# Performance work log

Measured on AMD Instinct MI355X. Metric: run time of the kernel, lower is better.

## Reference

```python
import jax, jax.numpy as jnp
import numpy as np
import math

HIDDEN = 2048
HEADS = 16
GROUPS = 4
HEAD_DIM = HIDDEN // HEADS  # 128
KV_DIM = GROUPS * HEAD_DIM  # 512
B, S = 2, 2048


def setup_inputs() -> dict:
    key = jax.random.key(0)
    ks = jax.random.split(key, 10)
    scale = 0.02
    return {
        "X": jax.random.normal(ks[0], (B, S, HIDDEN), dtype=jnp.float32),
        "attention_mask": jnp.ones((B, S), dtype=jnp.int32),
        "Wq": jax.random.normal(ks[1], (HIDDEN, HIDDEN), dtype=jnp.float32) * scale,
        "bq": jnp.zeros((HIDDEN,), dtype=jnp.float32),
        "Wk": jax.random.normal(ks[2], (HIDDEN, KV_DIM), dtype=jnp.float32) * scale,
        "bk": jnp.zeros((KV_DIM,), dtype=jnp.float32),
        "Wv": jax.random.normal(ks[3], (HIDDEN, KV_DIM), dtype=jnp.float32) * scale,
        "bv": jnp.zeros((KV_DIM,), dtype=jnp.float32),
        "Wo": jax.random.normal(ks[4], (HIDDEN, HIDDEN), dtype=jnp.float32) * scale,
        "bo": jnp.zeros((HIDDEN,), dtype=jnp.float32),
    }


def reference(X, attention_mask, Wq, bq, Wk, bk, Wv, bv, Wo, bo):
    b, s, _ = X.shape
    num_per_group = HEADS // GROUPS
    # projections
    Q = (X @ Wq + bq).reshape(b, s, HEADS, HEAD_DIM).transpose(0, 2, 1, 3)   # [b,H,s,d]
    K = (X @ Wk + bk).reshape(b, s, GROUPS, HEAD_DIM).transpose(0, 2, 1, 3)  # [b,G,s,d]
    V = (X @ Wv + bv).reshape(b, s, GROUPS, HEAD_DIM).transpose(0, 2, 1, 3)
    # torch .repeat(1, num_per_group, 1, 1) tiles group axis: [g0..gG-1, g0..gG-1, ...]
    K = jnp.tile(K, (1, num_per_group, 1, 1))  # [b,H,s,d]
    V = jnp.tile(V, (1, num_per_group, 1, 1))
    scores = jnp.einsum("bhqd,bhkd->bhqk", Q, K) / math.sqrt(HEAD_DIM)
    mask = attention_mask[:, None, None, :] == 0  # [b,1,1,s]
    scores = jnp.where(mask, jnp.float32(-jnp.inf), scores)
    attn = jax.nn.softmax(scores, axis=-1)
    out = jnp.einsum("bhqk,bhkd->bhqd", attn, V)  # [b,H,s,d]
    out = out.transpose(0, 2, 1, 3).reshape(b, s, HIDDEN)
    return out @ Wo + bo
```

## Files before the change

### kernel.cpp

```cpp
#include <hip/hip_runtime.h>
#include <hip/hip_bf16.h>


typedef __attribute__((ext_vector_type(8))) short short8;
typedef __attribute__((ext_vector_type(4))) short short4v;
typedef __attribute__((ext_vector_type(4))) float float4v;

#define C1F 0.12751743f
#define B0F -16.0f

#if defined(__has_builtin) && __has_builtin(__builtin_amdgcn_exp2f)
#define EXP2(x) __builtin_amdgcn_exp2f(x)
#else
#define EXP2(x) exp2f(x)
#endif

__device__ __forceinline__ short f2bf(float x) {
    __hip_bfloat16 h = __float2bfloat16(x);
    short s; __builtin_memcpy(&s, &h, sizeof(s)); return s;
}

__device__ __forceinline__ void gl16(const short* g, short* l) {
    __builtin_amdgcn_global_load_lds(
        (const __attribute__((address_space(1))) void*)g,
        (__attribute__((address_space(3))) void*)l, 16, 0, 0);
}

__global__ __launch_bounds__(256) void cvt_bf16_kernel(const float* __restrict__ in,
                                                       short* __restrict__ out, int n) {
    int i = (blockIdx.x * 256 + threadIdx.x) * 4;
    if (i >= n) return;
    float4 v = *(const float4*)(in + i);
    short4v o;
    o[0] = f2bf(v.x); o[1] = f2bf(v.y); o[2] = f2bf(v.z); o[3] = f2bf(v.w);
    *(short4v*)(out + i) = o;
}

__global__ __launch_bounds__(256) void transpose_cvt_kernel(const float* __restrict__ W,
                                                            short* __restrict__ Wt,
                                                            int K, int N) {
    __shared__ float tile[32][33];
    int n0 = blockIdx.x * 32, k0 = blockIdx.y * 32;
    int tx = threadIdx.x & 31, ty = threadIdx.x >> 5;
#pragma unroll
    for (int i = 0; i < 4; ++i) {
        int kk = ty + i * 8;
        tile[kk][tx] = W[(size_t)(k0 + kk) * N + n0 + tx];
    }
    __syncthreads();
#pragma unroll
    for (int i = 0; i < 4; ++i) {
        int nn = ty + i * 8;
        Wt[(size_t)(n0 + nn) * K + k0 + tx] = f2bf(tile[tx][nn]);
    }
}

__global__ __launch_bounds__(256) void gemm_dma_kernel(
    const short* __restrict__ A, const short* __restrict__ Bt,
    const float* __restrict__ b0, const float* __restrict__ b1, const float* __restrict__ b2,
    short* __restrict__ O0, short* __restrict__ O1, short* __restrict__ O2,
    float* __restrict__ Of, int K, int mode) {
    __shared__ short As[128 * 32];
    __shared__ short Bs[128 * 32];
    const int t = threadIdx.x, lane = t & 63, w = t >> 6;
    const int l15 = lane & 15, quad = lane >> 4;
    const int wm = (w & 1) * 64, wn = (w >> 1) * 64;
    const int m0 = blockIdx.y * 128, n0 = blockIdx.x * 128;
    const int r4 = lane >> 2, c8 = (lane & 3) * 8;
    const short* ga = A + (size_t)(m0 + w * 16 + r4) * K + c8;
    const short* gb = Bt + (size_t)(n0 + w * 16 + r4) * K + c8;
    short* lA = As + (w * 16) * 32;
    short* lB = Bs + (w * 16) * 32;

    float4v acc[4][4] = {};

    for (int k0 = 0; k0 < K; k0 += 32) {
        gl16(ga + k0, lA);
        gl16(ga + (size_t)64 * K + k0, lA + 64 * 32);
        gl16(gb + k0, lB);
        gl16(gb + (size_t)64 * K + k0, lB + 64 * 32);
        __syncthreads();
        short8 af[4], bfr[4];
#pragma unroll
        for (int i = 0; i < 4; ++i)
            af[i] = *(const short8*)(As + (wm + i * 16 + l15) * 32 + quad * 8);
#pragma unroll
        for (int j = 0; j < 4; ++j)
            bfr[j] = *(const short8*)(Bs + (wn + j * 16 + l15) * 32 + quad * 8);
#pragma unroll
        for (int i = 0; i < 4; ++i)
#pragma unroll
            for (int j = 0; j < 4; ++j)
                acc[i][j] = __builtin_amdgcn_mfma_f32_16x16x32_bf16(af[i], bfr[j], acc[i][j], 0, 0, 0);
        __syncthreads();
    }

#pragma unroll
    for (int i = 0; i < 4; ++i) {
#pragma unroll
        for (int j = 0; j < 4; ++j) {
            const int col = n0 + wn + j * 16 + l15;
            const int row0 = m0 + wm + i * 16 + quad * 4;
            if (mode == 1) {
                const float bc = b0[col];
#pragma unroll
                for (int r = 0; r < 4; ++r)
                    Of[(size_t)(row0 + r) * 2048 + col] = acc[i][j][r] + bc;
            } else if (col < 2048) {
                const float bc = b0[col];
#pragma unroll
                for (int r = 0; r < 4; ++r)
                    O0[(size_t)(row0 + r) * 2048 + col] = f2bf(acc[i][j][r] + bc);
            } else if (col < 2560) {
                const int c = col - 2048;
                const float bc = b1[c];
#pragma unroll
                for (int r = 0; r < 4; ++r)
                    O1[(size_t)(row0 + r) * 512 + c] = f2bf(acc[i][j][r] + bc);
            } else {
                const int c = col - 2560;
                const float bc = b2[c];
#pragma unroll
                for (int r = 0; r < 4; ++r)
                    O2[(size_t)c * 4096 + row0 + r] = f2bf(acc[i][j][r] + bc);
            }
        }
    }
}

__global__ __launch_bounds__(256, 2) void flash_kernel(
    const short* __restrict__ Qb, const short* __restrict__ Kb,
    const short* __restrict__ Vt, const int* __restrict__ mask,
    short* __restrict__ Ab) {
    __shared__ short Ks[64 * 136];
    __shared__ short Vs[128 * 72];
    __shared__ short Ps[4 * 32 * 72];
    __shared__ float mb[64];

    const int t = threadIdx.x;
    const int lane = t & 63, w = t >> 6;
    const int l15 = lane & 15, quad = lane >> 4;
    const int qt = blockIdx.x, g = blockIdx.y, b = blockIdx.z;
    const int h = g + 4 * w;
    const int q0 = qt * 32;

    short8 qf[2][4];
#pragma unroll
    for (int mi = 0; mi < 2; ++mi)
#pragma unroll
        for (int ks = 0; ks < 4; ++ks)
            qf[mi][ks] = *(const short8*)(Qb + (size_t)(b * 2048 + q0 + mi * 16 + l15) * 2048
                                          + h * 128 + ks * 32 + quad * 8);

    float4v o[2][8] = {};
    float rsum[2][4] = {};
    short* PsW = Ps + w * (32 * 72);
    const int psxr = ((l15 >> 3) & 1) << 4;

    const int kR = t >> 4, kC = (t & 15) * 8;
    const int vR = t >> 3, vC = (t & 7) * 8;
    const short* kg = Kb + (size_t)(b * 2048 + kR) * 512 + g * 128 + kC;
    const short* vg = Vt + (size_t)(g * 128 + vR) * 4096 + (size_t)b * 2048 + vC;

    short8 kv[4], vv[4];
    float mv = 0.f;

#define LOADT(KB)                                                                  \
    do {                                                                           \
        kv[0] = *(const short8*)(kg + (size_t)(KB) * 512);                         \
        kv[1] = *(const short8*)(kg + (size_t)((KB) + 16) * 512);                  \
        kv[2] = *(const short8*)(kg + (size_t)((KB) + 32) * 512);                  \
        kv[3] = *(const short8*)(kg + (size_t)((KB) + 48) * 512);                  \
        vv[0] = *(const short8*)(vg + (KB));                                       \
        vv[1] = *(const short8*)(vg + (size_t)32 * 4096 + (KB));                   \
        vv[2] = *(const short8*)(vg + (size_t)64 * 4096 + (KB));                   \
        vv[3] = *(const short8*)(vg + (size_t)96 * 4096 + (KB));                   \
        if (t < 64) mv = mask[b * 2048 + (KB) + t] ? B0F : -1e30f;                 \
    } while (0)

    LOADT(0);

    for (int kt = 0; kt < 32; ++kt) {
        __syncthreads();
#pragma unroll
        for (int i = 0; i < 4; ++i)
            *(short8*)(Ks + (kR + i * 16) * 136 + kC) = kv[i];
#pragma unroll
        for (int i = 0; i < 4; ++i)
            *(short8*)(Vs + (vR + i * 32) * 72 + vC) = vv[i];
        if (t < 64) mb[t] = mv;
        __syncthreads();

        if (kt + 1 < 32) LOADT((kt + 1) * 64);

        float4v s[2][4] = {};
        __builtin_amdgcn_s_setprio(1);
#pragma unroll
        for (int ks = 0; ks < 4; ++ks)
#pragma unroll
            for (int j = 0; j < 4; ++j) {
                short8 bk = *(const short8*)(Ks + (j * 16 + l15) * 136 + ks * 32 + quad * 8);
                s[0][j] = __builtin_amdgcn_mfma_f32_16x16x32_bf16(qf[0][ks], bk, s[0][j], 0, 0, 0);
                s[1][j] = __builtin_amdgcn_mfma_f32_16x16x32_bf16(qf[1][ks], bk, s[1][j], 0, 0, 0);
            }
        __builtin_amdgcn_s_setprio(0);
#pragma unroll
        for (int mi = 0; mi < 2; ++mi)
#pragma unroll
            for (int j = 0; j < 4; ++j) {
                const float mbias = mb[j * 16 + l15];
#pragma unroll
                for (int r = 0; r < 4; ++r) {
                    float p = EXP2(fmaf(s[mi][j][r], C1F, mbias));
                    rsum[mi][r] += p;
                    const int row = mi * 16 + quad * 4 + r;
                    PsW[row * 72 + ((j * 16 + l15) ^ (((row >> 3) & 1) << 4))] = f2bf(p);
                }
            }
        __builtin_amdgcn_s_setprio(1);
#pragma unroll
        for (int ks2 = 0; ks2 < 2; ++ks2) {
            short8 pa0 = *(const short8*)(PsW + l15 * 72 + ((ks2 * 32 + quad * 8) ^ psxr));
            short8 pa1 = *(const short8*)(PsW + (16 + l15) * 72 + ((ks2 * 32 + quad * 8) ^ psxr));
#pragma unroll
            for (int jj = 0; jj < 8; ++jj) {
                short8 bv = *(const short8*)(Vs + (jj * 16 + l15) * 72 + ks2 * 32 + quad * 8);
                o[0][jj] = __builtin_amdgcn_mfma_f32_16x16x32_bf16(pa0, bv, o[0][jj], 0, 0, 0);
                o[1][jj] = __builtin_amdgcn_mfma_f32_16x16x32_bf16(pa1, bv, o[1][jj], 0, 0, 0);
            }
        }
        __builtin_amdgcn_s_setprio(0);
    }
#undef LOADT

    float rinv[2][4];
#pragma unroll
    for (int mi = 0; mi < 2; ++mi)
#pragma unroll
        for (int r = 0; r < 4; ++r) {
            float v = rsum[mi][r];
            v += __shfl_xor(v, 1, 64); v += __shfl_xor(v, 2, 64);
            v += __shfl_xor(v, 4, 64); v += __shfl_xor(v, 8, 64);
            rinv[mi][r] = (v > 0.f) ? 1.f / v : 0.f;
        }
    const size_t ob = (size_t)(b * 2048 + q0) * 2048 + h * 128;
#pragma unroll
    for (int mi = 0; mi < 2; ++mi)
#pragma unroll
        for (int jj = 0; jj < 8; ++jj)
#pragma unroll
            for (int r = 0; r < 4; ++r)
                Ab[ob + (size_t)(mi * 16 + quad * 4 + r) * 2048 + jj * 16 + l15] =
                    f2bf(o[mi][jj][r] * rinv[mi][r]);
}

extern "C" void kernel_launch(void* const* d_in, const int* in_sizes, int n_in,
                              void* d_out, int out_size, void* d_ws, size_t ws_size,
                              hipStream_t stream) {
    (void)in_sizes; (void)n_in; (void)out_size; (void)ws_size;
    const float* X  = (const float*)d_in[0];
    const int* mask = (const int*)d_in[1];
    const float* Wq = (const float*)d_in[2];
    const float* bq = (const float*)d_in[3];
    const float* Wk = (const float*)d_in[4];
    const float* bk = (const float*)d_in[5];
    const float* Wv = (const float*)d_in[6];
    const float* bv = (const float*)d_in[7];
    const float* Wo = (const float*)d_in[8];
    const float* bo = (const float*)d_in[9];
    float* out = (float*)d_out;

    char* ws = (char*)d_ws;
    short* Xb     = (short*)(ws + 0);
    short* WqkvT  = (short*)(ws + 16777216);
    short* Wot    = (short*)(ws + 29360128);
    short* Qb     = (short*)(ws + 37748736);
    short* Kb     = (short*)(ws + 54525952);
    short* Vt     = (short*)(ws + 58720256);
    short* Ab     = Xb;

    const int M = 4096, HID = 2048, KV = 512;

    cvt_bf16_kernel<<<8192, 256, 0, stream>>>(X, Xb, M * HID);
    transpose_cvt_kernel<<<dim3(64, 64), 256, 0, stream>>>(Wq, WqkvT, HID, HID);
    transpose_cvt_kernel<<<dim3(16, 64), 256, 0, stream>>>(Wk, WqkvT + (size_t)2048 * 2048, HID, KV);
    transpose_cvt_kernel<<<dim3(16, 64), 256, 0, stream>>>(Wv, WqkvT + (size_t)2560 * 2048, HID, KV);
    transpose_cvt_kernel<<<dim3(64, 64), 256, 0, stream>>>(Wo, Wot, HID, HID);

    gemm_dma_kernel<<<dim3(24, 32), 256, 0, stream>>>(
        Xb, WqkvT, bq, bk, bv, Qb, Kb, Vt, nullptr, HID, 0);

    flash_kernel<<<dim3(64, 4, 2), 256, 0, stream>>>(Qb, Kb, Vt, mask, Ab);

    gemm_dma_kernel<<<dim3(16, 32), 256, 0, stream>>>(
        Ab, Wot, bo, nullptr, nullptr, nullptr, nullptr, nullptr, out, HID, 1);
}
```

Measured before the change: 355.6 us.

## Rewrite flash attention with 32x32 MFMA, register-resident P, double-buffered LDS

The attention kernel moves from 16x16x32 to 32x32x16 bf16 MFMA and computes S transposed, so the softmax probabilities stay in registers and feed the PV MFMA directly instead of passing through an LDS scratch buffer. K/V tiles are double-buffered in LDS, which drops one barrier per iteration. The mask becomes a wave ballot bitmask applied with selects. The projection epilogue writes V transposed in a permuted row order so it matches the new P register layout. The cost is more LDS for the second buffer and a heavier accumulator register footprint.

```diff
diff --git a/kernel.cpp b/kernel.cpp
--- a/kernel.cpp
+++ b/kernel.cpp
@@ -5,6 +5,7 @@
 typedef __attribute__((ext_vector_type(8))) short short8;
 typedef __attribute__((ext_vector_type(4))) short short4v;
 typedef __attribute__((ext_vector_type(4))) float float4v;
+typedef __attribute__((ext_vector_type(16))) float float16v;
 
 #define C1F 0.12751743f
 #define B0F -16.0f
@@ -120,9 +121,11 @@
             } else {
                 const int c = col - 2560;
                 const float bc = b2[c];
+                const int qsw = ((quad & 1) << 1) | (quad >> 1);
+                const int prow = m0 + wm + i * 16 + qsw * 4;
 #pragma unroll
                 for (int r = 0; r < 4; ++r)
-                    O2[(size_t)c * 4096 + row0 + r] = f2bf(acc[i][j][r] + bc);
+                    O2[(size_t)c * 4096 + prow + r] = f2bf(acc[i][j][r] + bc);
             }
         }
     }
@@ -132,30 +135,24 @@
     const short* __restrict__ Qb, const short* __restrict__ Kb,
     const short* __restrict__ Vt, const int* __restrict__ mask,
     short* __restrict__ Ab) {
-    __shared__ short Ks[64 * 136];
-    __shared__ short Vs[128 * 72];
-    __shared__ short Ps[4 * 32 * 72];
-    __shared__ float mb[64];
+    __shared__ short Ks[2][64 * 136];
+    __shared__ short Vs[2][128 * 72];
 
     const int t = threadIdx.x;
     const int lane = t & 63, w = t >> 6;
-    const int l15 = lane & 15, quad = lane >> 4;
+    const int l31 = lane & 31, hi = lane >> 5;
     const int qt = blockIdx.x, g = blockIdx.y, b = blockIdx.z;
     const int h = g + 4 * w;
     const int q0 = qt * 32;
 
-    short8 qf[2][4];
-#pragma unroll
-    for (int mi = 0; mi < 2; ++mi)
-#pragma unroll
-        for (int ks = 0; ks < 4; ++ks)
-            qf[mi][ks] = *(const short8*)(Qb + (size_t)(b * 2048 + q0 + mi * 16 + l15) * 2048
-                                          + h * 128 + ks * 32 + quad * 8);
-
-    float4v o[2][8] = {};
-    float rsum[2][4] = {};
-    short* PsW = Ps + w * (32 * 72);
-    const int psxr = ((l15 >> 3) & 1) << 4;
+    short8 qf[8];
+#pragma unroll
+    for (int dd = 0; dd < 8; ++dd)
+        qf[dd] = *(const short8*)(Qb + (size_t)(b * 2048 + q0 + l31) * 2048
+                                  + h * 128 + dd * 16 + hi * 8);
+
+    float16v o[4] = {};
+    float rsum = 0.f;
 
     const int kR = t >> 4, kC = (t & 15) * 8;
     const int vR = t >> 3, vC = (t & 7) * 8;
@@ -163,7 +160,7 @@
     const short* vg = Vt + (size_t)(g * 128 + vR) * 4096 + (size_t)b * 2048 + vC;
 
     short8 kv[4], vv[4];
-    float mv = 0.f;
+    int mvr = 1;
 
 #define LOADT(KB)                                                                  \
     do {                                                                           \
@@ -175,83 +172,102 @@
         vv[1] = *(const short8*)(vg + (size_t)32 * 4096 + (KB));                   \
         vv[2] = *(const short8*)(vg + (size_t)64 * 4096 + (KB));                   \
         vv[3] = *(const short8*)(vg + (size_t)96 * 4096 + (KB));                   \
-        if (t < 64) mv = mask[b * 2048 + (KB) + t] ? B0F : -1e30f;                 \
+        mvr = mask[b * 2048 + (KB) + lane];                                        \
     } while (0)
 
+#define STAGE(BUF)                                                                 \
+    do {                                                                           \
+        _Pragma("unroll")                                                          \
+        for (int i_ = 0; i_ < 4; ++i_)                                             \
+            *(short8*)(&Ks[BUF][(kR + i_ * 16) * 136 + kC]) = kv[i_];              \
+        _Pragma("unroll")                                                          \
+        for (int i_ = 0; i_ < 4; ++i_)                                             \
+            *(short8*)(&Vs[BUF][(vR + i_ * 32) * 72 + vC]) = vv[i_];               \
+    } while (0)
+
     LOADT(0);
+    STAGE(0);
+    unsigned long long bits = __ballot(mvr != 0);
+    LOADT(64);
+    __syncthreads();
+
+    int cur = 0;
+    unsigned long long bits_next = bits;
 
     for (int kt = 0; kt < 32; ++kt) {
+        if (kt + 1 < 32) {
+            STAGE(cur ^ 1);
+            bits_next = __ballot(mvr != 0);
+            if (kt + 2 < 32) LOADT((kt + 2) * 64);
+        }
+        const short* Ksb = &Ks[cur][0];
+        const short* Vsb = &Vs[cur][0];
+
+        float16v st0 = {}, st1 = {};
+        __builtin_amdgcn_s_setprio(1);
+#pragma unroll
+        for (int dd = 0; dd < 8; ++dd) {
+            short8 kf0 = *(const short8*)(Ksb + l31 * 136 + dd * 16 + hi * 8);
+            short8 kf1 = *(const short8*)(Ksb + (32 + l31) * 136 + dd * 16 + hi * 8);
+            st0 = __builtin_amdgcn_mfma_f32_32x32x16_bf16(kf0, qf[dd], st0, 0, 0, 0);
+            st1 = __builtin_amdgcn_mfma_f32_32x32x16_bf16(kf1, qf[dd], st1, 0, 0, 0);
+        }
+        __builtin_amdgcn_s_setprio(0);
+
+        const unsigned int mlo = ((unsigned int)bits) >> (4 * hi);
+        const unsigned int mhi = ((unsigned int)(bits >> 32)) >> (4 * hi);
+#pragma unroll
+        for (int e = 0; e < 16; ++e) {
+            const int koff = (e & 3) + 8 * (e >> 2);
+            float p0 = EXP2(fmaf(st0[e], C1F, B0F));
+            float p1 = EXP2(fmaf(st1[e], C1F, B0F));
+            p0 = ((mlo >> koff) & 1) ? p0 : 0.f;
+            p1 = ((mhi >> koff) & 1) ? p1 : 0.f;
+            rsum += p0 + p1;
+            st0[e] = p0; st1[e] = p1;
+        }
+
+        __builtin_amdgcn_s_setprio(1);
+#pragma unroll
+        for (int cc = 0; cc < 4; ++cc) {
+            short8 pa;
+#pragma unroll
+            for (int e = 0; e < 8; ++e) {
+                const float pv_ = (cc & 2) ? st1[(cc & 1) * 8 + e] : st0[(cc & 1) * 8 + e];
+                pa[e] = f2bf(pv_);
+            }
+#pragma unroll
+            for (int db = 0; db < 4; ++db) {
+                short8 vb = *(const short8*)(Vsb + (db * 32 + l31) * 72 + cc * 16 + hi * 8);
+                o[db] = __builtin_amdgcn_mfma_f32_32x32x16_bf16(pa, vb, o[db], 0, 0, 0);
+            }
+        }
+        __builtin_amdgcn_s_setprio(0);
+
         __syncthreads();
-#pragma unroll
-        for (int i = 0; i < 4; ++i)
-            *(short8*)(Ks + (kR + i * 16) * 136 + kC) = kv[i];
-#pragma unroll
-        for (int i = 0; i < 4; ++i)
-            *(short8*)(Vs + (vR + i * 32) * 72 + vC) = vv[i];
-        if (t < 64) mb[t] = mv;
-        __syncthreads();
-
-        if (kt + 1 < 32) LOADT((kt + 1) * 64);
-
-        float4v s[2][4] = {};
-        __builtin_amdgcn_s_setprio(1);
-#pragma unroll
-        for (int ks = 0; ks < 4; ++ks)
-#pragma unroll
-            for (int j = 0; j < 4; ++j) {
-                short8 bk = *(const short8*)(Ks + (j * 16 + l15) * 136 + ks * 32 + quad * 8);
-                s[0][j] = __builtin_amdgcn_mfma_f32_16x16x32_bf16(qf[0][ks], bk, s[0][j], 0, 0, 0);
-                s[1][j] = __builtin_amdgcn_mfma_f32_16x16x32_bf16(qf[1][ks], bk, s[1][j], 0, 0, 0);
-            }
-        __builtin_amdgcn_s_setprio(0);
-#pragma unroll
-        for (int mi = 0; mi < 2; ++mi)
-#pragma unroll
-            for (int j = 0; j < 4; ++j) {
-                const float mbias = mb[j * 16 + l15];
-#pragma unroll
-                for (int r = 0; r < 4; ++r) {
-                    float p = EXP2(fmaf(s[mi][j][r], C1F, mbias));
-                    rsum[mi][r] += p;
-                    const int row = mi * 16 + quad * 4 + r;
-                    PsW[row * 72 + ((j * 16 + l15) ^ (((row >> 3) & 1) << 4))] = f2bf(p);
-                }
-            }
-        __builtin_amdgcn_s_setprio(1);
-#pragma unroll
-        for (int ks2 = 0; ks2 < 2; ++ks2) {
-            short8 pa0 = *(const short8*)(PsW + l15 * 72 + ((ks2 * 32 + quad * 8) ^ psxr));
-            short8 pa1 = *(const short8*)(PsW + (16 + l15) * 72 + ((ks2 * 32 + quad * 8) ^ psxr));
-#pragma unroll
-            for (int jj = 0; jj < 8; ++jj) {
-                short8 bv = *(const short8*)(Vs + (jj * 16 + l15) * 72 + ks2 * 32 + quad * 8);
-                o[0][jj] = __builtin_amdgcn_mfma_f32_16x16x32_bf16(pa0, bv, o[0][jj], 0, 0, 0);
-                o[1][jj] = __builtin_amdgcn_mfma_f32_16x16x32_bf16(pa1, bv, o[1][jj], 0, 0, 0);
-            }
-        }
-        __builtin_amdgcn_s_setprio(0);
+        bits = bits_next;
+        cur ^= 1;
     }
 #undef LOADT
-
-    float rinv[2][4];
-#pragma unroll
-    for (int mi = 0; mi < 2; ++mi)
-#pragma unroll
-        for (int r = 0; r < 4; ++r) {
-            float v = rsum[mi][r];
-            v += __shfl_xor(v, 1, 64); v += __shfl_xor(v, 2, 64);
-            v += __shfl_xor(v, 4, 64); v += __shfl_xor(v, 8, 64);
-            rinv[mi][r] = (v > 0.f) ? 1.f / v : 0.f;
-        }
+#undef STAGE
+
+    rsum += __shfl_xor(rsum, 32, 64);
+    const float rinv = (rsum > 0.f) ? 1.f / rsum : 0.f;
+    float rq[16];
+#pragma unroll
+    for (int e = 0; e < 16; ++e) {
+        const int koff = (e & 3) + 8 * (e >> 2);
+        rq[e] = __shfl(rinv, koff + 4 * hi, 64);
+    }
     const size_t ob = (size_t)(b * 2048 + q0) * 2048 + h * 128;
 #pragma unroll
-    for (int mi = 0; mi < 2; ++mi)
-#pragma unroll
-        for (int jj = 0; jj < 8; ++jj)
-#pragma unroll
-            for (int r = 0; r < 4; ++r)
-                Ab[ob + (size_t)(mi * 16 + quad * 4 + r) * 2048 + jj * 16 + l15] =
-                    f2bf(o[mi][jj][r] * rinv[mi][r]);
+    for (int db = 0; db < 4; ++db)
+#pragma unroll
+        for (int e = 0; e < 16; ++e) {
+            const int koff = (e & 3) + 8 * (e >> 2);
+            Ab[ob + (size_t)(koff + 4 * hi) * 2048 + db * 32 + l31] =
+                f2bf(o[db][e] * rq[e]);
+        }
 }
 
 extern "C" void kernel_launch(void* const* d_in, const int* in_sizes, int n_in,
```

Result: faster. 343.4 us (-3.4%).
